# Optimization experiments

Hardware: AMD Instinct MI355X
Metric: run time of the kernel (lower is better)

The kernel has to match this reference:

```python
import jax, jax.numpy as jnp
import numpy as np

B, S, D, T = 32, 2048, 128, 8  # batch, seq, input_size, num_trans


def setup_inputs() -> dict:
    key = jax.random.key(0)
    k0, k1, k2, k3 = jax.random.split(key, 4)
    return {
        "input_data": jax.random.normal(k0, (B, S, D), dtype=jnp.float32),
        # nn.Linear(D, D) weights per transform, stacked: [T, D, D]
        "Wx": jax.random.normal(k1, (T, D, D), dtype=jnp.float32) / np.sqrt(D).astype(np.float32),
        "bx": jax.random.normal(k2, (T, D), dtype=jnp.float32) * 0.01,
        # torch.rand init in original
        "p_vectors": jax.random.uniform(k3, (T, 1, D), dtype=jnp.float32),
    }


def reference(input_data, Wx, bx, p_vectors):
    # Batched version of the Python loop of per-transform Linears.
    # torch Linear computes x @ W.T + b -> contract last dim of x with last dim of W.
    transformed = jnp.einsum('bsd,ted->tbse', input_data, Wx) + bx[:, None, None, :]  # [T,B,S,D]

    # Cosine-similarity gating against prototype vectors p_vectors [T,1,D].
    x_norm = jnp.linalg.norm(input_data, axis=2, keepdims=True)[None]        # [1,B,S,1]
    p_norm = jnp.linalg.norm(p_vectors, axis=2, keepdims=True)[:, None]      # [T,1,1,1]
    dot = jnp.sum(input_data[None] * p_vectors[:, None], axis=3, keepdims=True)  # [T,B,S,1]
    cos = dot / (x_norm * p_norm)
    sim = jax.nn.softmax(cos, axis=0)  # softmax over the T transforms

    # Weighted combine + residual (is_y=False path).
    return jnp.sum(sim * transformed, axis=0) + input_data  # [B,S,D]
```

## Files before the change

### kernel.cpp

```cpp
#include <hip/hip_runtime.h>

#define Bq 32
#define Sq 2048
#define Dq 128
#define Tq 8
#define Mq (Bq * Sq)

typedef __attribute__((ext_vector_type(8))) short bf16x8;
typedef __attribute__((ext_vector_type(4))) float f32x4;

static __device__ __forceinline__ unsigned short f2bf(float f) {
    unsigned int u = __float_as_uint(f);
    unsigned int r = (u + 0x7FFFu + ((u >> 16) & 1u)) >> 16;
    return (unsigned short)r;
}

__global__ void prep_kernel(const float* __restrict__ W, unsigned short* __restrict__ wsw) {
    int i = blockIdx.x * 256 + threadIdx.x;
    int j    = i & 7;
    int lane = (i >> 3) & 63;
    int k    = (i >> 9) & 3;
    int n    = (i >> 11) & 7;
    int t    = i >> 14;
    int e = n * 16 + (lane & 15);
    int d = k * 32 + (lane >> 4) * 8 + j;
    wsw[i] = f2bf(W[(t * 128 + e) * 128 + d]);
}

__global__ __launch_bounds__(256, 2) void main_kernel(const float* __restrict__ x,
                                                      const unsigned short* __restrict__ wsw,
                                                      const float* __restrict__ bx,
                                                      const float* __restrict__ p,
                                                      float* __restrict__ out) {
    __shared__ unsigned short xs[64][136];
    __shared__ float simT[Tq][64];
    __shared__ float bxl[Tq][128];
    __shared__ float4 p4[Tq][32];
    __shared__ float pinv[Tq];

    int tid = threadIdx.x;
    size_t m0 = (size_t)blockIdx.x * 64;

    int r = tid >> 2;
    int h = tid & 3;

    const float4* xg = reinterpret_cast<const float4*>(x + (m0 + r) * 128) + h * 8;
    float4 xv[8];
    #pragma unroll
    for (int j = 0; j < 8; j++) xv[j] = xg[j];

    reinterpret_cast<float4*>(&p4[0][0])[tid] = reinterpret_cast<const float4*>(p)[tid];
    reinterpret_cast<float4*>(&bxl[0][0])[tid] = reinterpret_cast<const float4*>(bx)[tid];
    __syncthreads();
    if (tid < Tq) {
        float s = 0.f;
        #pragma unroll
        for (int i = 0; i < 32; i++) {
            float4 v = p4[tid][i];
            s += v.x * v.x + v.y * v.y + v.z * v.z + v.w * v.w;
        }
        pinv[tid] = rsqrtf(s);
    }
    __syncthreads();

    float dot[Tq];
    #pragma unroll
    for (int t = 0; t < Tq; t++) dot[t] = 0.f;
    float ssq = 0.f;
    #pragma unroll
    for (int j = 0; j < 8; j++) {
        float4 v = xv[j];
        ssq += v.x * v.x + v.y * v.y + v.z * v.z + v.w * v.w;
        #pragma unroll
        for (int t = 0; t < Tq; t++) {
            float4 pv = p4[t][h * 8 + j];
            dot[t] += v.x * pv.x + v.y * pv.y + v.z * pv.z + v.w * pv.w;
        }
    }
    #pragma unroll
    for (int jj = 0; jj < 4; jj++) {
        float4 v0 = xv[2 * jj], v1 = xv[2 * jj + 1];
        bf16x8 b;
        b[0] = (short)f2bf(v0.x); b[1] = (short)f2bf(v0.y);
        b[2] = (short)f2bf(v0.z); b[3] = (short)f2bf(v0.w);
        b[4] = (short)f2bf(v1.x); b[5] = (short)f2bf(v1.y);
        b[6] = (short)f2bf(v1.z); b[7] = (short)f2bf(v1.w);
        *reinterpret_cast<bf16x8*>(&xs[r][h * 32 + jj * 8]) = b;
    }
    ssq += __shfl_xor(ssq, 1);
    ssq += __shfl_xor(ssq, 2);
    #pragma unroll
    for (int t = 0; t < Tq; t++) {
        dot[t] += __shfl_xor(dot[t], 1);
        dot[t] += __shfl_xor(dot[t], 2);
    }
    float xinv = rsqrtf(ssq);
    float c[Tq], mx = -1e30f;
    #pragma unroll
    for (int t = 0; t < Tq; t++) {
        c[t] = dot[t] * xinv * pinv[t];
        mx = fmaxf(mx, c[t]);
    }
    float sum = 0.f;
    #pragma unroll
    for (int t = 0; t < Tq; t++) { c[t] = __expf(c[t] - mx); sum += c[t]; }
    float inv = 1.f / sum;
    #pragma unroll
    for (int i = 0; i < 2; i++) simT[h * 2 + i][r] = c[h * 2 + i] * inv;
    __syncthreads();

    int wid  = tid >> 6;
    int lane = tid & 63;
    int l16  = lane & 15;
    int quad = lane >> 4;
    int ncol = wid * 32;
    int nt0  = wid * 2;

    bf16x8 a[4][4];
    #pragma unroll
    for (int mt = 0; mt < 4; mt++)
        #pragma unroll
        for (int k = 0; k < 4; k++)
            a[mt][k] = *reinterpret_cast<const bf16x8*>(&xs[mt * 16 + l16][k * 32 + quad * 8]);

    f32x4 o[4][2] = {};

    const bf16x8* wbase = reinterpret_cast<const bf16x8*>(wsw);
    bf16x8 bf[2][4];
    #pragma unroll
    for (int k = 0; k < 4; k++)
        bf[0][k] = wbase[((size_t)(0 * 8 + nt0) * 4 + k) * 64 + lane];

    #pragma unroll 1
    for (int t = 0; t < Tq; t++) {
        f32x4 s4[4];
        #pragma unroll
        for (int mt = 0; mt < 4; mt++)
            s4[mt] = *reinterpret_cast<const f32x4*>(&simT[t][mt * 16 + quad * 4]);

        #pragma unroll
        for (int n = 0; n < 2; n++) {
            const int cur = n;
            {
                const int n2 = n ^ 1;
                int t2 = (n == 1) ? ((t + 1) & 7) : t;
                #pragma unroll
                for (int k = 0; k < 4; k++)
                    bf[cur ^ 1][k] = wbase[((size_t)(t2 * 8 + nt0 + n2) * 4 + k) * 64 + lane];
            }
            float bias = bxl[t][ncol + n * 16 + l16];
            f32x4 y0 = {bias, bias, bias, bias};
            f32x4 y[4] = {y0, y0, y0, y0};
            __builtin_amdgcn_s_setprio(1);
            #pragma unroll
            for (int k = 0; k < 4; k++)
                #pragma unroll
                for (int mt = 0; mt < 4; mt++)
                    y[mt] = __builtin_amdgcn_mfma_f32_16x16x32_bf16(a[mt][k], bf[cur][k], y[mt], 0, 0, 0);
            __builtin_amdgcn_s_setprio(0);
            #pragma unroll
            for (int mt = 0; mt < 4; mt++)
                #pragma unroll
                for (int rr = 0; rr < 4; rr++)
                    o[mt][n][rr] += s4[mt][rr] * y[mt][rr];
        }
    }

    #pragma unroll
    for (int mt = 0; mt < 4; mt++)
        #pragma unroll
        for (int rr = 0; rr < 4; rr++) {
            size_t row = m0 + mt * 16 + quad * 4 + rr;
            #pragma unroll
            for (int n = 0; n < 2; n++) {
                size_t idx = row * 128 + ncol + n * 16 + l16;
                float xr = __builtin_nontemporal_load(&x[idx]);
                __builtin_nontemporal_store(xr + o[mt][n][rr], &out[idx]);
            }
        }
}

extern "C" void kernel_launch(void* const* d_in, const int* in_sizes, int n_in,
                              void* d_out, int out_size, void* d_ws, size_t ws_size,
                              hipStream_t stream) {
    const float* x   = (const float*)d_in[0];
    const float* Wx  = (const float*)d_in[1];
    const float* bx  = (const float*)d_in[2];
    const float* p   = (const float*)d_in[3];
    float* out = (float*)d_out;

    unsigned short* wsw = (unsigned short*)d_ws;

    prep_kernel<<<dim3(512), dim3(256), 0, stream>>>(Wx, wsw);
    main_kernel<<<dim3(Mq / 64), dim3(256), 0, stream>>>(x, wsw, bx, p, out);
}
```

Measured before the change: 105.8 us.

## Coalesce weight prep through LDS and deepen weight prefetch pipeline

```diff
diff --git a/kernel.cpp b/kernel.cpp
--- a/kernel.cpp
+++ b/kernel.cpp
@@ -7,6 +7,7 @@
 #define Mq (Bq * Sq)
 
 typedef __attribute__((ext_vector_type(8))) short bf16x8;
+typedef __attribute__((ext_vector_type(8))) unsigned short u16x8;
 typedef __attribute__((ext_vector_type(4))) float f32x4;
 
 static __device__ __forceinline__ unsigned short f2bf(float f) {
@@ -15,16 +16,34 @@
     return (unsigned short)r;
 }
 
-__global__ void prep_kernel(const float* __restrict__ W, unsigned short* __restrict__ wsw) {
-    int i = blockIdx.x * 256 + threadIdx.x;
-    int j    = i & 7;
-    int lane = (i >> 3) & 63;
-    int k    = (i >> 9) & 3;
-    int n    = (i >> 11) & 7;
-    int t    = i >> 14;
-    int e = n * 16 + (lane & 15);
-    int d = k * 32 + (lane >> 4) * 8 + j;
-    wsw[i] = f2bf(W[(t * 128 + e) * 128 + d]);
+__global__ __launch_bounds__(256) void prep_kernel(const float* __restrict__ W,
+                                                   unsigned short* __restrict__ wsw) {
+    __shared__ unsigned short lds[32][132];
+    int tid = threadIdx.x;
+    int b = blockIdx.x;
+    int rl = tid >> 3;
+    int c0 = (tid & 7) * 16;
+    const float4* src = reinterpret_cast<const float4*>(W + ((size_t)b * 32 + rl) * 128 + c0);
+    #pragma unroll
+    for (int q = 0; q < 4; q++) {
+        float4 v = src[q];
+        lds[rl][c0 + q * 4 + 0] = f2bf(v.x);
+        lds[rl][c0 + q * 4 + 1] = f2bf(v.y);
+        lds[rl][c0 + q * 4 + 2] = f2bf(v.z);
+        lds[rl][c0 + q * 4 + 3] = f2bf(v.w);
+    }
+    __syncthreads();
+    u16x8* dst = reinterpret_cast<u16x8*>(wsw) + (size_t)b * 512 + tid * 2;
+    #pragma unroll
+    for (int u = 0; u < 2; u++) {
+        int oo   = tid * 2 + u;
+        int lane = oo & 63;
+        int kk   = (oo >> 6) & 3;
+        int nn   = oo >> 8;
+        int e    = nn * 16 + (lane & 15);
+        int d    = kk * 32 + (lane >> 4) * 8;
+        dst[u] = *reinterpret_cast<const u16x8*>(&lds[e][d]);
+    }
 }
 
 __global__ __launch_bounds__(256, 2) void main_kernel(const float* __restrict__ x,
@@ -44,6 +63,27 @@
     int r = tid >> 2;
     int h = tid & 3;
 
+    int wid  = tid >> 6;
+    int lane = tid & 63;
+    int l16  = lane & 15;
+    int quad = lane >> 4;
+    int ncol = wid * 32;
+    int nt0  = wid * 2;
+
+    const bf16x8* wbase = reinterpret_cast<const bf16x8*>(wsw);
+    bf16x8 bA[8], bB[8];
+
+    #define BF_LOAD(buf, tv)                                                          \
+    {                                                                                 \
+        _Pragma("unroll")                                                             \
+        for (int n2 = 0; n2 < 2; n2++) {                                              \
+            _Pragma("unroll")                                                         \
+            for (int kk = 0; kk < 4; kk++)                                            \
+                buf[n2 * 4 + kk] =                                                    \
+                    wbase[((size_t)((tv) * 8 + nt0 + n2) * 4 + kk) * 64 + lane];      \
+        }                                                                             \
+    }
+
     const float4* xg = reinterpret_cast<const float4*>(x + (m0 + r) * 128) + h * 8;
     float4 xv[8];
     #pragma unroll
@@ -51,6 +91,9 @@
 
     reinterpret_cast<float4*>(&p4[0][0])[tid] = reinterpret_cast<const float4*>(p)[tid];
     reinterpret_cast<float4*>(&bxl[0][0])[tid] = reinterpret_cast<const float4*>(bx)[tid];
+
+    BF_LOAD(bA, 0)
+
     __syncthreads();
     if (tid < Tq) {
         float s = 0.f;
@@ -109,13 +152,6 @@
     for (int i = 0; i < 2; i++) simT[h * 2 + i][r] = c[h * 2 + i] * inv;
     __syncthreads();
 
-    int wid  = tid >> 6;
-    int lane = tid & 63;
-    int l16  = lane & 15;
-    int quad = lane >> 4;
-    int ncol = wid * 32;
-    int nt0  = wid * 2;
-
     bf16x8 a[4][4];
     #pragma unroll
     for (int mt = 0; mt < 4; mt++)
@@ -125,45 +161,41 @@
 
     f32x4 o[4][2] = {};
 
-    const bf16x8* wbase = reinterpret_cast<const bf16x8*>(wsw);
-    bf16x8 bf[2][4];
-    #pragma unroll
-    for (int k = 0; k < 4; k++)
-        bf[0][k] = wbase[((size_t)(0 * 8 + nt0) * 4 + k) * 64 + lane];
+    #define COMPUTE(tv, buf)                                                          \
+    {                                                                                 \
+        f32x4 s4[4];                                                                  \
+        _Pragma("unroll")                                                             \
+        for (int mt = 0; mt < 4; mt++)                                                \
+            s4[mt] = *reinterpret_cast<const f32x4*>(&simT[tv][mt * 16 + quad * 4]);  \
+        _Pragma("unroll")                                                             \
+        for (int n = 0; n < 2; n++) {                                                 \
+            float bias = bxl[tv][ncol + n * 16 + l16];                                \
+            f32x4 y0v = {bias, bias, bias, bias};                                     \
+            f32x4 y[4] = {y0v, y0v, y0v, y0v};                                        \
+            __builtin_amdgcn_s_setprio(1);                                            \
+            _Pragma("unroll")                                                         \
+            for (int kk = 0; kk < 4; kk++) {                                          \
+                _Pragma("unroll")                                                     \
+                for (int mt = 0; mt < 4; mt++)                                        \
+                    y[mt] = __builtin_amdgcn_mfma_f32_16x16x32_bf16(                  \
+                        a[mt][kk], buf[n * 4 + kk], y[mt], 0, 0, 0);                  \
+            }                                                                         \
+            __builtin_amdgcn_s_setprio(0);                                            \
+            _Pragma("unroll")                                                         \
+            for (int mt = 0; mt < 4; mt++) {                                          \
+                _Pragma("unroll")                                                     \
+                for (int rr = 0; rr < 4; rr++)                                        \
+                    o[mt][n][rr] += s4[mt][rr] * y[mt][rr];                           \
+            }                                                                         \
+        }                                                                             \
+    }
 
     #pragma unroll 1
-    for (int t = 0; t < Tq; t++) {
-        f32x4 s4[4];
-        #pragma unroll
-        for (int mt = 0; mt < 4; mt++)
-            s4[mt] = *reinterpret_cast<const f32x4*>(&simT[t][mt * 16 + quad * 4]);
-
-        #pragma unroll
-        for (int n = 0; n < 2; n++) {
-            const int cur = n;
-            {
-                const int n2 = n ^ 1;
-                int t2 = (n == 1) ? ((t + 1) & 7) : t;
-                #pragma unroll
-                for (int k = 0; k < 4; k++)
-                    bf[cur ^ 1][k] = wbase[((size_t)(t2 * 8 + nt0 + n2) * 4 + k) * 64 + lane];
-            }
-            float bias = bxl[t][ncol + n * 16 + l16];
-            f32x4 y0 = {bias, bias, bias, bias};
-            f32x4 y[4] = {y0, y0, y0, y0};
-            __builtin_amdgcn_s_setprio(1);
-            #pragma unroll
-            for (int k = 0; k < 4; k++)
-                #pragma unroll
-                for (int mt = 0; mt < 4; mt++)
-                    y[mt] = __builtin_amdgcn_mfma_f32_16x16x32_bf16(a[mt][k], bf[cur][k], y[mt], 0, 0, 0);
-            __builtin_amdgcn_s_setprio(0);
-            #pragma unroll
-            for (int mt = 0; mt < 4; mt++)
-                #pragma unroll
-                for (int rr = 0; rr < 4; rr++)
-                    o[mt][n][rr] += s4[mt][rr] * y[mt][rr];
-        }
+    for (int tt = 0; tt < 4; tt++) {
+        BF_LOAD(bB, 2 * tt + 1)
+        COMPUTE(2 * tt, bA)
+        BF_LOAD(bA, (2 * tt + 2) & 7)
+        COMPUTE(2 * tt + 1, bB)
     }
 
     #pragma unroll
@@ -191,6 +223,6 @@
 
     unsigned short* wsw = (unsigned short*)d_ws;
 
-    prep_kernel<<<dim3(512), dim3(256), 0, stream>>>(Wx, wsw);
+    prep_kernel<<<dim3(32), dim3(256), 0, stream>>>(Wx, wsw);
     main_kernel<<<dim3(Mq / 64), dim3(256), 0, stream>>>(x, wsw, bx, p, out);
 }
```

New measurement: 106.8 us. No clear change (+0.9%).

## Retile waves to 2x2 M/N layout, raise occupancy, coalesce weight prep via LDS

Applied to the files above, without the earlier changes.

```diff
diff --git a/kernel.cpp b/kernel.cpp
--- a/kernel.cpp
+++ b/kernel.cpp
@@ -7,6 +7,7 @@
 #define Mq (Bq * Sq)
 
 typedef __attribute__((ext_vector_type(8))) short bf16x8;
+typedef __attribute__((ext_vector_type(8))) unsigned short u16x8;
 typedef __attribute__((ext_vector_type(4))) float f32x4;
 
 static __device__ __forceinline__ unsigned short f2bf(float f) {
@@ -15,19 +16,32 @@
     return (unsigned short)r;
 }
 
-__global__ void prep_kernel(const float* __restrict__ W, unsigned short* __restrict__ wsw) {
-    int i = blockIdx.x * 256 + threadIdx.x;
-    int j    = i & 7;
-    int lane = (i >> 3) & 63;
-    int k    = (i >> 9) & 3;
-    int n    = (i >> 11) & 7;
-    int t    = i >> 14;
-    int e = n * 16 + (lane & 15);
-    int d = k * 32 + (lane >> 4) * 8 + j;
-    wsw[i] = f2bf(W[(t * 128 + e) * 128 + d]);
-}
-
-__global__ __launch_bounds__(256, 2) void main_kernel(const float* __restrict__ x,
+__global__ __launch_bounds__(256) void prep_kernel(const float* __restrict__ W,
+                                                   unsigned short* __restrict__ wsw) {
+    __shared__ unsigned short lds[16][132];
+    int tid = threadIdx.x;
+    int b = blockIdx.x;
+    int rl = tid >> 4;
+    int c0 = (tid & 15) * 8;
+    const float4* src = reinterpret_cast<const float4*>(W + ((size_t)b * 16 + rl) * 128 + c0);
+    #pragma unroll
+    for (int q = 0; q < 2; q++) {
+        float4 v = src[q];
+        lds[rl][c0 + q * 4 + 0] = f2bf(v.x);
+        lds[rl][c0 + q * 4 + 1] = f2bf(v.y);
+        lds[rl][c0 + q * 4 + 2] = f2bf(v.z);
+        lds[rl][c0 + q * 4 + 3] = f2bf(v.w);
+    }
+    __syncthreads();
+    int lane = tid & 63;
+    int kk   = tid >> 6;
+    int e    = lane & 15;
+    int d    = kk * 32 + (lane >> 4) * 8;
+    u16x8* dst = reinterpret_cast<u16x8*>(wsw) + (size_t)b * 256 + tid;
+    *dst = *reinterpret_cast<const u16x8*>(&lds[e][d]);
+}
+
+__global__ __launch_bounds__(256, 4) void main_kernel(const float* __restrict__ x,
                                                       const unsigned short* __restrict__ wsw,
                                                       const float* __restrict__ bx,
                                                       const float* __restrict__ p,
@@ -44,6 +58,17 @@
     int r = tid >> 2;
     int h = tid & 3;
 
+    int wid  = tid >> 6;
+    int lane = tid & 63;
+    int l16  = lane & 15;
+    int quad = lane >> 4;
+    int mrow = (wid >> 1) * 32;
+    int ncol = (wid & 1) * 64;
+    int nt0  = (wid & 1) * 4;
+
+    const bf16x8* wbase = reinterpret_cast<const bf16x8*>(wsw);
+    bf16x8 bf[2][4];
+
     const float4* xg = reinterpret_cast<const float4*>(x + (m0 + r) * 128) + h * 8;
     float4 xv[8];
     #pragma unroll
@@ -51,6 +76,11 @@
 
     reinterpret_cast<float4*>(&p4[0][0])[tid] = reinterpret_cast<const float4*>(p)[tid];
     reinterpret_cast<float4*>(&bxl[0][0])[tid] = reinterpret_cast<const float4*>(bx)[tid];
+
+    #pragma unroll
+    for (int kk = 0; kk < 4; kk++)
+        bf[0][kk] = wbase[((size_t)(0 * 8 + nt0) * 4 + kk) * 64 + lane];
+
     __syncthreads();
     if (tid < Tq) {
         float s = 0.f;
@@ -109,70 +139,54 @@
     for (int i = 0; i < 2; i++) simT[h * 2 + i][r] = c[h * 2 + i] * inv;
     __syncthreads();
 
-    int wid  = tid >> 6;
-    int lane = tid & 63;
-    int l16  = lane & 15;
-    int quad = lane >> 4;
-    int ncol = wid * 32;
-    int nt0  = wid * 2;
-
-    bf16x8 a[4][4];
-    #pragma unroll
-    for (int mt = 0; mt < 4; mt++)
-        #pragma unroll
-        for (int k = 0; k < 4; k++)
-            a[mt][k] = *reinterpret_cast<const bf16x8*>(&xs[mt * 16 + l16][k * 32 + quad * 8]);
-
-    f32x4 o[4][2] = {};
-
-    const bf16x8* wbase = reinterpret_cast<const bf16x8*>(wsw);
-    bf16x8 bf[2][4];
-    #pragma unroll
-    for (int k = 0; k < 4; k++)
-        bf[0][k] = wbase[((size_t)(0 * 8 + nt0) * 4 + k) * 64 + lane];
+    bf16x8 a[2][4];
+    #pragma unroll
+    for (int mt = 0; mt < 2; mt++)
+        #pragma unroll
+        for (int kk = 0; kk < 4; kk++)
+            a[mt][kk] = *reinterpret_cast<const bf16x8*>(&xs[mrow + mt * 16 + l16][kk * 32 + quad * 8]);
+
+    f32x4 o[2][4] = {};
 
     #pragma unroll 1
     for (int t = 0; t < Tq; t++) {
-        f32x4 s4[4];
-        #pragma unroll
-        for (int mt = 0; mt < 4; mt++)
-            s4[mt] = *reinterpret_cast<const f32x4*>(&simT[t][mt * 16 + quad * 4]);
-
-        #pragma unroll
-        for (int n = 0; n < 2; n++) {
-            const int cur = n;
+        #pragma unroll
+        for (int n = 0; n < 4; n++) {
+            const int cur = n & 1;
             {
-                const int n2 = n ^ 1;
-                int t2 = (n == 1) ? ((t + 1) & 7) : t;
+                const int n2 = (n + 1) & 3;
+                int t2 = (n == 3) ? ((t + 1) & 7) : t;
                 #pragma unroll
-                for (int k = 0; k < 4; k++)
-                    bf[cur ^ 1][k] = wbase[((size_t)(t2 * 8 + nt0 + n2) * 4 + k) * 64 + lane];
+                for (int kk = 0; kk < 4; kk++)
+                    bf[cur ^ 1][kk] = wbase[((size_t)(t2 * 8 + nt0 + n2) * 4 + kk) * 64 + lane];
             }
             float bias = bxl[t][ncol + n * 16 + l16];
-            f32x4 y0 = {bias, bias, bias, bias};
-            f32x4 y[4] = {y0, y0, y0, y0};
+            f32x4 y0v = {bias, bias, bias, bias};
+            f32x4 y[2] = {y0v, y0v};
             __builtin_amdgcn_s_setprio(1);
             #pragma unroll
-            for (int k = 0; k < 4; k++)
+            for (int kk = 0; kk < 4; kk++)
                 #pragma unroll
-                for (int mt = 0; mt < 4; mt++)
-                    y[mt] = __builtin_amdgcn_mfma_f32_16x16x32_bf16(a[mt][k], bf[cur][k], y[mt], 0, 0, 0);
+                for (int mt = 0; mt < 2; mt++)
+                    y[mt] = __builtin_amdgcn_mfma_f32_16x16x32_bf16(a[mt][kk], bf[cur][kk], y[mt], 0, 0, 0);
             __builtin_amdgcn_s_setprio(0);
             #pragma unroll
-            for (int mt = 0; mt < 4; mt++)
+            for (int mt = 0; mt < 2; mt++) {
+                f32x4 s4 = *reinterpret_cast<const f32x4*>(&simT[t][mrow + mt * 16 + quad * 4]);
                 #pragma unroll
                 for (int rr = 0; rr < 4; rr++)
-                    o[mt][n][rr] += s4[mt][rr] * y[mt][rr];
-        }
-    }
-
-    #pragma unroll
-    for (int mt = 0; mt < 4; mt++)
+                    o[mt][n][rr] += s4[rr] * y[mt][rr];
+            }
+        }
+    }
+
+    #pragma unroll
+    for (int mt = 0; mt < 2; mt++)
         #pragma unroll
         for (int rr = 0; rr < 4; rr++) {
-            size_t row = m0 + mt * 16 + quad * 4 + rr;
+            size_t row = m0 + mrow + mt * 16 + quad * 4 + rr;
             #pragma unroll
-            for (int n = 0; n < 2; n++) {
+            for (int n = 0; n < 4; n++) {
                 size_t idx = row * 128 + ncol + n * 16 + l16;
                 float xr = __builtin_nontemporal_load(&x[idx]);
                 __builtin_nontemporal_store(xr + o[mt][n][rr], &out[idx]);
@@ -191,6 +205,6 @@
 
     unsigned short* wsw = (unsigned short*)d_ws;
 
-    prep_kernel<<<dim3(512), dim3(256), 0, stream>>>(Wx, wsw);
+    prep_kernel<<<dim3(64), dim3(256), 0, stream>>>(Wx, wsw);
     main_kernel<<<dim3(Mq / 64), dim3(256), 0, stream>>>(x, wsw, bx, p, out);
 }
```

Result: slower. 114.6 us (+8.3%).
